# Performance work log

Measured on AMD Instinct MI355X. Metric: run time of the kernel, lower is better.

Reference implementation:

```python
import jax, jax.numpy as jnp
import numpy as np

NEG_INF = -9e15  # matches the source's -9000000000000000.0 mask fill
ALPHA = 0.2      # leaky_relu negative slope


def setup_inputs() -> dict:
    key = jax.random.key(0)
    k1, k2, k3, k4 = jax.random.split(key, 4)
    B, N, C_IN, C_OUT, H = 2, 2048, 128, 128, 16
    c = C_OUT // H  # 8 per-head features; equals H//2 so source's a-slice is consistent
    node_feats = jax.random.normal(k1, (B, N, C_IN), dtype=jnp.float32)
    # random 0/1 adjacency with self-loops
    adj = jax.random.randint(k2, (B, N, N), 0, 2).astype(jnp.float32)
    adj = jnp.maximum(adj, jnp.eye(N, dtype=jnp.float32)[None])
    # glorot-uniform-ish params
    W = jax.random.normal(k3, (C_IN, H * c), dtype=jnp.float32) * np.sqrt(2.0 / (C_IN + H * c))
    b = jnp.zeros((H * c,), dtype=jnp.float32)
    a = jax.random.normal(k4, (H, 2 * c), dtype=jnp.float32) * np.sqrt(2.0 / (H + 2 * c))
    return {"node_feats": node_feats, "adj_matrix": adj, "W": W, "b": b, "a": a}


def reference(node_feats, adj_matrix, W, b, a):
    B, N = node_feats.shape[:2]
    H = a.shape[0]
    c = a.shape[1] // 2
    # projection + split into heads: [B, N, H, c]
    h = (node_feats @ W + b).reshape(B, N, H, c)
    # additive attention halves (source slices a along last axis)
    logit_parent = jnp.einsum('bnhc,hc->bnh', h, a[:, :c])
    logit_child = jnp.einsum('bnhc,hc->bnh', h, a[:, c:])
    # dense broadcast-add logits: [B, N(i), N(j), H]
    attn_logits = logit_parent[:, :, None, :] + logit_child[:, None, :, :]
    attn_logits = jax.nn.leaky_relu(attn_logits, negative_slope=ALPHA)
    attn_logits = jnp.where(adj_matrix[..., None] == 1.0, attn_logits, NEG_INF)
    attn_probs = jax.nn.softmax(attn_logits, axis=2)  # over source nodes j
    out = jnp.einsum('bijh,bjhc->bihc', attn_probs, h)
    out = out.reshape(B, N, H * c)  # concat_heads=True
    return out, adj_matrix
```

## Files before the change

### kernel.cpp

```cpp
#include <hip/hip_runtime.h>
#include <hip/hip_bf16.h>


#define B_   2
#define N_   2048
#define CIN_ 128
#define H_   16

typedef _Float16 h2  __attribute__((ext_vector_type(2)));
typedef _Float16 v8h __attribute__((ext_vector_type(8)));
typedef float    v4f __attribute__((ext_vector_type(4)));

#define SC6 0.015625f

__device__ inline h2 pk_f16(float a, float b) {
  return __builtin_bit_cast(h2, __builtin_amdgcn_cvt_pkrtz(a, b));
}
__device__ inline unsigned as_u32(h2 v) { return __builtin_bit_cast(unsigned, v); }
__device__ inline h2 as_h2(unsigned u) { return __builtin_bit_cast(h2, u); }

__device__ inline unsigned mask4(float4 f) {
  unsigned r = (unsigned)f.x | ((unsigned)f.y << 8) |
               ((unsigned)f.z << 16) | ((unsigned)f.w << 24);
  return (r << 8) - r;
}

__global__ __launch_bounds__(128) void proj_kernel(
    const float* __restrict__ nf, const float* __restrict__ W,
    const float* __restrict__ bias, const float* __restrict__ a,
    unsigned* __restrict__ hQ, unsigned* __restrict__ qI,
    float* __restrict__ lpT, unsigned* __restrict__ ones) {
  const int row0 = blockIdx.x * 4;
  const int t    = threadIdx.x;
  if (blockIdx.x == 0) {
    ones[t] = 0x3C003C00u; ones[t + 128] = 0x3C003C00u;
    ones[t + 256] = 0x3C003C00u; ones[t + 384] = 0x3C003C00u;
  }
  __shared__ float sNf[4][CIN_];
  ((float4*)&sNf[0][0])[t] = ((const float4*)(nf + (long)row0 * CIN_))[t];
  __syncthreads();
  float acc[4];
  const float bv = bias[t];
#pragma unroll
  for (int r = 0; r < 4; ++r) acc[r] = bv;
#pragma unroll 8
  for (int k = 0; k < CIN_; ++k) {
    const float w = W[k * 128 + t];
#pragma unroll
    for (int r = 0; r < 4; ++r) acc[r] = fmaf(sNf[r][k], w, acc[r]);
  }
  const int h = t >> 3, kc = t & 7;
  const int b = row0 >> 11, n0 = row0 & (N_ - 1);
  const int bh = b * H_ + h;
  const int cdw = n0 >> 1;
  uint2 hv;
  hv.x = as_u32(pk_f16(acc[0], acc[1]));
  hv.y = as_u32(pk_f16(acc[2], acc[3]));
  *(uint2*)(hQ + ((long)(bh * 8 + kc)) * (N_ / 2) + cdw) = hv;

  const float ap = a[h * 16 + kc], ac = a[h * 16 + 8 + kc];
  float lpv[4], lcv[4];
#pragma unroll
  for (int r = 0; r < 4; ++r) {
    float x = acc[r] * ap, y = acc[r] * ac;
#pragma unroll
    for (int s = 1; s < 8; s <<= 1) {
      x += __shfl_xor(x, s);
      y += __shfl_xor(y, s);
    }
    lpv[r] = x; lcv[r] = y;
  }
  if (kc == 0) {
    float4 l0 = {lpv[0], lpv[1], lpv[2], lpv[3]};
    *(float4*)(lpT + (long)bh * N_ + n0) = l0;
    uint2 q1, q2;
    q1.x = as_u32(pk_f16(__expf(lcv[0]) * SC6, __expf(lcv[1]) * SC6));
    q1.y = as_u32(pk_f16(__expf(lcv[2]) * SC6, __expf(lcv[3]) * SC6));
    q2.x = as_u32(pk_f16(__expf(0.2f * lcv[0]) * SC6, __expf(0.2f * lcv[1]) * SC6));
    q2.y = as_u32(pk_f16(__expf(0.2f * lcv[2]) * SC6, __expf(0.2f * lcv[3]) * SC6));
    const int addr = bh * 2048 + (cdw >> 4) * 32 + ((cdw >> 2) & 3) * 8;
    const int off  = cdw & 3;
    *(uint2*)(qI + addr + off)     = q1;
    *(uint2*)(qI + addr + 4 + off) = q2;
  }
}

__global__ __launch_bounds__(256) void attn_kernel(
    const float* __restrict__ adj, const unsigned* __restrict__ hQ,
    const unsigned* __restrict__ qI, const float* __restrict__ lpT,
    const unsigned* __restrict__ ones, float* __restrict__ out,
    float* __restrict__ adj_out) {
  const int hg   = blockIdx.x & 3;
  const int it   = (blockIdx.x >> 2) & 63;
  const int b    = blockIdx.x >> 8;
  const int i0   = it * 32;
  const int t    = threadIdx.x;
  const int w    = t >> 6;
  const int lane = t & 63;
  const int m    = lane & 15;
  const int q    = lane >> 4;
  const int h    = hg * 4 + w;
  const int bh   = b * H_ + h;

  __shared__ uint2 sAm[8192];

  const int  tm = t & 15, tq = t >> 4;
  const long abase = ((long)(b * N_) + i0) * N_;

  float4 fa[2][4], fb[2][4];
  auto STAGE_LOAD = [&](int ss) {
#pragma unroll
    for (int u = 0; u < 2; ++u)
#pragma unroll
      for (int k = 0; k < 4; ++k) {
        const int qc  = ss * 64 + k * 16 + tq;
        const int col = qc * 8;
        const float* ap = adj + abase + (long)(u * 16 + tm) * N_ + col;
        fa[u][k] = *(const float4*)(ap);
        fb[u][k] = *(const float4*)(ap + 4);
      }
  };
  auto STAGE_WRITE = [&](int ss) {
    const bool docopy = (ss == hg);
#pragma unroll
    for (int u = 0; u < 2; ++u)
#pragma unroll
      for (int k = 0; k < 4; ++k) {
        uint2 mv;
        mv.x = mask4(fa[u][k]); mv.y = mask4(fb[u][k]);
        sAm[u * 4096 + ss * 1024 + k * 256 + t] = mv;
        if (docopy) {
          const int qc  = ss * 64 + k * 16 + tq;
          const int col = qc * 8;
          float* op = adj_out + abase + (long)(u * 16 + tm) * N_ + col;
          *(float4*)(op)     = fa[u][k];
          *(float4*)(op + 4) = fb[u][k];
        }
      }
  };

  const float lpa = lpT[(long)bh * N_ + i0 + m];
  const float lpb = lpT[(long)bh * N_ + i0 + 16 + m];
  const float e1a = __expf(lpa) * SC6, e2a = __expf(0.2f * lpa) * SC6;
  const float e1b = __expf(lpb) * SC6, e2b = __expf(0.2f * lpb) * SC6;
  const h2 P1a = pk_f16(e1a, e1a), P2a = pk_f16(e2a, e2a);
  const h2 P1b = pk_f16(e1b, e1b), P2b = pk_f16(e2b, e2b);

  const unsigned* qp = qI + bh * 2048 + q * 8;
  const unsigned hmask = (m < 8) ? ~0u : 0u;
  const unsigned* hp = (m < 8)
      ? hQ + ((long)(bh * 8 + m)) * (N_ / 2) + q * 4
      : ones + q * 4;

  uint4 bq1[2], bq2[2], bhq[2];
  bq1[0] = *(const uint4*)(qp);       bq2[0] = *(const uint4*)(qp + 4);
  bq1[1] = *(const uint4*)(qp + 32);  bq2[1] = *(const uint4*)(qp + 36);
  bhq[0] = *(const uint4*)(hp);
  bhq[1] = *(const uint4*)(hp + (16 & hmask));

  v4f acc0 = {0.f, 0.f, 0.f, 0.f};
  v4f acc1 = {0.f, 0.f, 0.f, 0.f};

  STAGE_LOAD(0);
  STAGE_WRITE(0);
  __syncthreads();

  for (int s = 0; s < 4; ++s) {
    if (s < 3) STAGE_LOAD(s + 1);
#pragma unroll
    for (int cc = 0; cc < 16; ++cc) {
      const int ch = s * 16 + cc;
      const int p  = ch & 1;
      const uint4 nq1 = *(const uint4*)(qp + (ch + 2) * 32);
      const uint4 nq2 = *(const uint4*)(qp + (ch + 2) * 32 + 4);
      const uint4 nhq = *(const uint4*)(hp + (((ch + 2) * 16) & hmask));

      const uint2 Mv0 = sAm[ch * 64 + lane];
      const uint2 Mv1 = sAm[4096 + ch * 64 + lane];
      const unsigned m0a = __builtin_amdgcn_perm(Mv0.x, Mv0.x, 0x01010000u);
      const unsigned m0b = __builtin_amdgcn_perm(Mv0.x, Mv0.x, 0x03030202u);
      const unsigned m0c = __builtin_amdgcn_perm(Mv0.y, Mv0.y, 0x01010000u);
      const unsigned m0d = __builtin_amdgcn_perm(Mv0.y, Mv0.y, 0x03030202u);
      const unsigned m1a = __builtin_amdgcn_perm(Mv1.x, Mv1.x, 0x01010000u);
      const unsigned m1b = __builtin_amdgcn_perm(Mv1.x, Mv1.x, 0x03030202u);
      const unsigned m1c = __builtin_amdgcn_perm(Mv1.y, Mv1.y, 0x01010000u);
      const unsigned m1d = __builtin_amdgcn_perm(Mv1.y, Mv1.y, 0x03030202u);

      const uint4 q1 = bq1[p], q2 = bq2[p];
      const h2 Q1x = as_h2(q1.x), Q1y = as_h2(q1.y), Q1z = as_h2(q1.z), Q1w = as_h2(q1.w);
      const h2 Q2x = as_h2(q2.x), Q2y = as_h2(q2.y), Q2z = as_h2(q2.z), Q2w = as_h2(q2.w);
      const v8h bf = __builtin_bit_cast(v8h, bhq[p]);

      const uint4 af0 = {
        as_u32(__builtin_elementwise_max(P1a * Q1x, P2a * Q2x)) & m0a,
        as_u32(__builtin_elementwise_max(P1a * Q1y, P2a * Q2y)) & m0b,
        as_u32(__builtin_elementwise_max(P1a * Q1z, P2a * Q2z)) & m0c,
        as_u32(__builtin_elementwise_max(P1a * Q1w, P2a * Q2w)) & m0d};
      acc0 = __builtin_amdgcn_mfma_f32_16x16x32_f16(
          __builtin_bit_cast(v8h, af0), bf, acc0, 0, 0, 0);
      const uint4 af1 = {
        as_u32(__builtin_elementwise_max(P1b * Q1x, P2b * Q2x)) & m1a,
        as_u32(__builtin_elementwise_max(P1b * Q1y, P2b * Q2y)) & m1b,
        as_u32(__builtin_elementwise_max(P1b * Q1z, P2b * Q2z)) & m1c,
        as_u32(__builtin_elementwise_max(P1b * Q1w, P2b * Q2w)) & m1d};
      acc1 = __builtin_amdgcn_mfma_f32_16x16x32_f16(
          __builtin_bit_cast(v8h, af1), bf, acc1, 0, 0, 0);

      bq1[p] = nq1; bq2[p] = nq2; bhq[p] = nhq;
    }
    if (s < 3) { STAGE_WRITE(s + 1); __syncthreads(); }
  }

#pragma unroll
  for (int u = 0; u < 2; ++u) {
    const v4f av = u ? acc1 : acc0;
#pragma unroll
    for (int r = 0; r < 4; ++r) {
      const float sden = __shfl(av[r], (lane & 48) | 8);
      if (m < 8) {
        const long gi = ((long)(b * N_ + i0 + u * 16 + q * 4 + r)) * H_ + h;
        out[gi * 8 + m] = av[r] / sden;
      }
    }
  }
}

extern "C" void kernel_launch(void* const* d_in, const int* in_sizes, int n_in,
                              void* d_out, int out_size, void* d_ws, size_t ws_size,
                              hipStream_t stream) {
  const float* nf   = (const float*)d_in[0];
  const float* adj  = (const float*)d_in[1];
  const float* W    = (const float*)d_in[2];
  const float* bias = (const float*)d_in[3];
  const float* a    = (const float*)d_in[4];

  float* out     = (float*)d_out;
  float* adj_out = out + (long)B_ * N_ * H_ * 8;

  unsigned* ws   = (unsigned*)d_ws;
  unsigned* hQ   = ws;
  unsigned* qI   = ws + 262144;
  float*    lpT  = (float*)(ws + 327680);
  unsigned* ones = ws + 393216;

  hipLaunchKernelGGL(proj_kernel, dim3(B_ * N_ / 4), dim3(128), 0, stream,
                     nf, W, bias, a, hQ, qI, lpT, ones);
  hipLaunchKernelGGL(attn_kernel, dim3(B_ * 64 * 4), dim3(256), 0,
                     stream, adj, hQ, qI, lpT, ones, out, adj_out);
}
```

Baseline: 139.5 us.

## Halve row tile per block, double grid, double-buffer adjacency masks with swizzled block order

Each block now handles 16 query rows instead of 32, so the grid grows from 512 to 1024 blocks and shared memory shrinks from 64KB to 8KB. Adjacency masks are staged in 8 smaller double-buffered chunks instead of holding the whole strip. Block indices are remapped so that neighbouring launch slots land on different row tiles, and launch bounds ask for 4 blocks per CU. The intent is higher occupancy and better latency hiding on the adjacency stream. The cost is that the per-node q/h operand loads and exp setup are now amortised over half as many rows, and there are more barriers per block.

```diff
diff --git a/kernel.cpp b/kernel.cpp
--- a/kernel.cpp
+++ b/kernel.cpp
@@ -85,15 +85,16 @@
   }
 }
 
-__global__ __launch_bounds__(256) void attn_kernel(
+__global__ __launch_bounds__(256, 4) void attn_kernel(
     const float* __restrict__ adj, const unsigned* __restrict__ hQ,
     const unsigned* __restrict__ qI, const float* __restrict__ lpT,
     const unsigned* __restrict__ ones, float* __restrict__ out,
     float* __restrict__ adj_out) {
-  const int hg   = blockIdx.x & 3;
-  const int it   = (blockIdx.x >> 2) & 63;
-  const int b    = blockIdx.x >> 8;
-  const int i0   = it * 32;
+  const int L    = (blockIdx.x & 7) * 128 + (blockIdx.x >> 3);
+  const int hg   = L & 3;
+  const int it   = (L >> 2) & 127;
+  const int b    = L >> 9;
+  const int i0   = it * 16;
   const int t    = threadIdx.x;
   const int w    = t >> 6;
   const int lane = t & 63;
@@ -102,49 +103,39 @@
   const int h    = hg * 4 + w;
   const int bh   = b * H_ + h;
 
-  __shared__ uint2 sAm[8192];
-
-  const int  tm = t & 15, tq = t >> 4;
-  const long abase = ((long)(b * N_) + i0) * N_;
-
-  float4 fa[2][4], fb[2][4];
+  __shared__ uint2 sAm[1024];
+
+  const int  tm = t & 15, cg = t >> 4;
+  const int  chl = cg >> 1, qh = (cg & 1) * 2;
+  const long abase = ((long)(b * N_) + i0 + tm) * N_ + cg * 16;
+  const bool owner_even = (hg == 0) | (hg == 1) | (hg == 2) | (hg == 3);
+
+  float4 f0, f1, f2, f3;
   auto STAGE_LOAD = [&](int ss) {
-#pragma unroll
-    for (int u = 0; u < 2; ++u)
-#pragma unroll
-      for (int k = 0; k < 4; ++k) {
-        const int qc  = ss * 64 + k * 16 + tq;
-        const int col = qc * 8;
-        const float* ap = adj + abase + (long)(u * 16 + tm) * N_ + col;
-        fa[u][k] = *(const float4*)(ap);
-        fb[u][k] = *(const float4*)(ap + 4);
-      }
+    const float* ap = adj + abase + ss * 256;
+    f0 = *(const float4*)(ap);
+    f1 = *(const float4*)(ap + 4);
+    f2 = *(const float4*)(ap + 8);
+    f3 = *(const float4*)(ap + 12);
   };
   auto STAGE_WRITE = [&](int ss) {
-    const bool docopy = (ss == hg);
-#pragma unroll
-    for (int u = 0; u < 2; ++u)
-#pragma unroll
-      for (int k = 0; k < 4; ++k) {
-        uint2 mv;
-        mv.x = mask4(fa[u][k]); mv.y = mask4(fb[u][k]);
-        sAm[u * 4096 + ss * 1024 + k * 256 + t] = mv;
-        if (docopy) {
-          const int qc  = ss * 64 + k * 16 + tq;
-          const int col = qc * 8;
-          float* op = adj_out + abase + (long)(u * 16 + tm) * N_ + col;
-          *(float4*)(op)     = fa[u][k];
-          *(float4*)(op + 4) = fb[u][k];
-        }
-      }
+    const int buf = (ss & 1) * 512;
+    uint2 mv0; mv0.x = mask4(f0); mv0.y = mask4(f1);
+    uint2 mv1; mv1.x = mask4(f2); mv1.y = mask4(f3);
+    sAm[buf + chl * 64 + qh * 16 + tm]       = mv0;
+    sAm[buf + chl * 64 + (qh + 1) * 16 + tm] = mv1;
+    if (hg == (ss & 3)) {
+      float* op = adj_out + abase + ss * 256;
+      *(float4*)(op)      = f0;
+      *(float4*)(op + 4)  = f1;
+      *(float4*)(op + 8)  = f2;
+      *(float4*)(op + 12) = f3;
+    }
   };
 
-  const float lpa = lpT[(long)bh * N_ + i0 + m];
-  const float lpb = lpT[(long)bh * N_ + i0 + 16 + m];
-  const float e1a = __expf(lpa) * SC6, e2a = __expf(0.2f * lpa) * SC6;
-  const float e1b = __expf(lpb) * SC6, e2b = __expf(0.2f * lpb) * SC6;
-  const h2 P1a = pk_f16(e1a, e1a), P2a = pk_f16(e2a, e2a);
-  const h2 P1b = pk_f16(e1b, e1b), P2b = pk_f16(e2b, e2b);
+  const float lp  = lpT[(long)bh * N_ + i0 + m];
+  const float e1  = __expf(lp) * SC6, e2 = __expf(0.2f * lp) * SC6;
+  const h2 P1 = pk_f16(e1, e1), P2 = pk_f16(e2, e2);
 
   const unsigned* qp = qI + bh * 2048 + q * 8;
   const unsigned hmask = (m < 8) ? ~0u : 0u;
@@ -158,71 +149,53 @@
   bhq[0] = *(const uint4*)(hp);
   bhq[1] = *(const uint4*)(hp + (16 & hmask));
 
-  v4f acc0 = {0.f, 0.f, 0.f, 0.f};
-  v4f acc1 = {0.f, 0.f, 0.f, 0.f};
+  v4f acc = {0.f, 0.f, 0.f, 0.f};
 
   STAGE_LOAD(0);
   STAGE_WRITE(0);
   __syncthreads();
 
-  for (int s = 0; s < 4; ++s) {
-    if (s < 3) STAGE_LOAD(s + 1);
-#pragma unroll
-    for (int cc = 0; cc < 16; ++cc) {
-      const int ch = s * 16 + cc;
+  for (int s = 0; s < 8; ++s) {
+    if (s < 7) STAGE_LOAD(s + 1);
+    const int buf = (s & 1) * 512;
+#pragma unroll
+    for (int cc = 0; cc < 8; ++cc) {
+      const int ch = s * 8 + cc;
       const int p  = ch & 1;
       const uint4 nq1 = *(const uint4*)(qp + (ch + 2) * 32);
       const uint4 nq2 = *(const uint4*)(qp + (ch + 2) * 32 + 4);
       const uint4 nhq = *(const uint4*)(hp + (((ch + 2) * 16) & hmask));
 
-      const uint2 Mv0 = sAm[ch * 64 + lane];
-      const uint2 Mv1 = sAm[4096 + ch * 64 + lane];
-      const unsigned m0a = __builtin_amdgcn_perm(Mv0.x, Mv0.x, 0x01010000u);
-      const unsigned m0b = __builtin_amdgcn_perm(Mv0.x, Mv0.x, 0x03030202u);
-      const unsigned m0c = __builtin_amdgcn_perm(Mv0.y, Mv0.y, 0x01010000u);
-      const unsigned m0d = __builtin_amdgcn_perm(Mv0.y, Mv0.y, 0x03030202u);
-      const unsigned m1a = __builtin_amdgcn_perm(Mv1.x, Mv1.x, 0x01010000u);
-      const unsigned m1b = __builtin_amdgcn_perm(Mv1.x, Mv1.x, 0x03030202u);
-      const unsigned m1c = __builtin_amdgcn_perm(Mv1.y, Mv1.y, 0x01010000u);
-      const unsigned m1d = __builtin_amdgcn_perm(Mv1.y, Mv1.y, 0x03030202u);
+      const uint2 Mv = sAm[buf + cc * 64 + lane];
+      const unsigned ma = __builtin_amdgcn_perm(Mv.x, Mv.x, 0x01010000u);
+      const unsigned mb = __builtin_amdgcn_perm(Mv.x, Mv.x, 0x03030202u);
+      const unsigned mc = __builtin_amdgcn_perm(Mv.y, Mv.y, 0x01010000u);
+      const unsigned md = __builtin_amdgcn_perm(Mv.y, Mv.y, 0x03030202u);
 
       const uint4 q1 = bq1[p], q2 = bq2[p];
-      const h2 Q1x = as_h2(q1.x), Q1y = as_h2(q1.y), Q1z = as_h2(q1.z), Q1w = as_h2(q1.w);
-      const h2 Q2x = as_h2(q2.x), Q2y = as_h2(q2.y), Q2z = as_h2(q2.z), Q2w = as_h2(q2.w);
       const v8h bf = __builtin_bit_cast(v8h, bhq[p]);
-
-      const uint4 af0 = {
-        as_u32(__builtin_elementwise_max(P1a * Q1x, P2a * Q2x)) & m0a,
-        as_u32(__builtin_elementwise_max(P1a * Q1y, P2a * Q2y)) & m0b,
-        as_u32(__builtin_elementwise_max(P1a * Q1z, P2a * Q2z)) & m0c,
-        as_u32(__builtin_elementwise_max(P1a * Q1w, P2a * Q2w)) & m0d};
-      acc0 = __builtin_amdgcn_mfma_f32_16x16x32_f16(
-          __builtin_bit_cast(v8h, af0), bf, acc0, 0, 0, 0);
-      const uint4 af1 = {
-        as_u32(__builtin_elementwise_max(P1b * Q1x, P2b * Q2x)) & m1a,
-        as_u32(__builtin_elementwise_max(P1b * Q1y, P2b * Q2y)) & m1b,
-        as_u32(__builtin_elementwise_max(P1b * Q1z, P2b * Q2z)) & m1c,
-        as_u32(__builtin_elementwise_max(P1b * Q1w, P2b * Q2w)) & m1d};
-      acc1 = __builtin_amdgcn_mfma_f32_16x16x32_f16(
-          __builtin_bit_cast(v8h, af1), bf, acc1, 0, 0, 0);
+      const uint4 af = {
+        as_u32(__builtin_elementwise_max(P1 * as_h2(q1.x), P2 * as_h2(q2.x))) & ma,
+        as_u32(__builtin_elementwise_max(P1 * as_h2(q1.y), P2 * as_h2(q2.y))) & mb,
+        as_u32(__builtin_elementwise_max(P1 * as_h2(q1.z), P2 * as_h2(q2.z))) & mc,
+        as_u32(__builtin_elementwise_max(P1 * as_h2(q1.w), P2 * as_h2(q2.w))) & md};
+      acc = __builtin_amdgcn_mfma_f32_16x16x32_f16(
+          __builtin_bit_cast(v8h, af), bf, acc, 0, 0, 0);
 
       bq1[p] = nq1; bq2[p] = nq2; bhq[p] = nhq;
     }
-    if (s < 3) { STAGE_WRITE(s + 1); __syncthreads(); }
-  }
-
-#pragma unroll
-  for (int u = 0; u < 2; ++u) {
-    const v4f av = u ? acc1 : acc0;
-#pragma unroll
-    for (int r = 0; r < 4; ++r) {
-      const float sden = __shfl(av[r], (lane & 48) | 8);
-      if (m < 8) {
-        const long gi = ((long)(b * N_ + i0 + u * 16 + q * 4 + r)) * H_ + h;
-        out[gi * 8 + m] = av[r] / sden;
-      }
-    }
-  }
+    if (s < 7) { STAGE_WRITE(s + 1); __syncthreads(); }
+  }
+
+#pragma unroll
+  for (int r = 0; r < 4; ++r) {
+    const float sden = __shfl(acc[r], (lane & 48) | 8);
+    if (m < 8) {
+      const long gi = ((long)(b * N_ + i0 + q * 4 + r)) * H_ + h;
+      out[gi * 8 + m] = acc[r] / sden;
+    }
+  }
+  (void)owner_even;
 }
 
 extern "C" void kernel_launch(void* const* d_in, const int* in_sizes, int n_in,
@@ -245,6 +218,6 @@
 
   hipLaunchKernelGGL(proj_kernel, dim3(B_ * N_ / 4), dim3(128), 0, stream,
                      nf, W, bias, a, hQ, qI, lpT, ones);
-  hipLaunchKernelGGL(attn_kernel, dim3(B_ * 64 * 4), dim3(256), 0,
+  hipLaunchKernelGGL(attn_kernel, dim3(1024), dim3(256), 0,
                      stream, adj, hQ, qI, lpT, ones, out, adj_out);
 }
```

New measurement: 146.5 us. 5.1% more time.

## Double-buffer adjacency and query tiles in LDS with interleaved prefetch

Applied to the files above, without the earlier changes.

The attention kernel now double-buffers both the adjacency mask and the per-head query-exponent vectors in shared memory. Loads for the next 512-column chunk are split into four sub-stages spread across the MFMA loop, with sched barriers to keep them in place. It also adds an occupancy hint of two blocks per CU and remaps block indices so neighbouring blocks are spread across XCDs. The aim is to hide global load latency behind compute and to cut register pressure from the per-thread query prefetch, at the cost of an extra __syncthreads per chunk and more LDS traffic.

```diff
diff --git a/kernel.cpp b/kernel.cpp
--- a/kernel.cpp
+++ b/kernel.cpp
@@ -85,58 +85,64 @@
   }
 }
 
-__global__ __launch_bounds__(256) void attn_kernel(
+__global__ __launch_bounds__(256, 2) void attn_kernel(
     const float* __restrict__ adj, const unsigned* __restrict__ hQ,
     const unsigned* __restrict__ qI, const float* __restrict__ lpT,
     const unsigned* __restrict__ ones, float* __restrict__ out,
     float* __restrict__ adj_out) {
-  const int hg   = blockIdx.x & 3;
-  const int it   = (blockIdx.x >> 2) & 63;
-  const int b    = blockIdx.x >> 8;
-  const int i0   = it * 32;
-  const int t    = threadIdx.x;
-  const int w    = t >> 6;
-  const int lane = t & 63;
-  const int m    = lane & 15;
-  const int q    = lane >> 4;
-  const int h    = hg * 4 + w;
-  const int bh   = b * H_ + h;
-
-  __shared__ uint2 sAm[8192];
-
-  const int  tm = t & 15, tq = t >> 4;
-  const long abase = ((long)(b * N_) + i0) * N_;
-
-  float4 fa[2][4], fb[2][4];
-  auto STAGE_LOAD = [&](int ss) {
-#pragma unroll
-    for (int u = 0; u < 2; ++u)
-#pragma unroll
-      for (int k = 0; k < 4; ++k) {
-        const int qc  = ss * 64 + k * 16 + tq;
-        const int col = qc * 8;
-        const float* ap = adj + abase + (long)(u * 16 + tm) * N_ + col;
-        fa[u][k] = *(const float4*)(ap);
-        fb[u][k] = *(const float4*)(ap + 4);
-      }
-  };
-  auto STAGE_WRITE = [&](int ss) {
-    const bool docopy = (ss == hg);
-#pragma unroll
-    for (int u = 0; u < 2; ++u)
-#pragma unroll
-      for (int k = 0; k < 4; ++k) {
-        uint2 mv;
-        mv.x = mask4(fa[u][k]); mv.y = mask4(fb[u][k]);
-        sAm[u * 4096 + ss * 1024 + k * 256 + t] = mv;
-        if (docopy) {
-          const int qc  = ss * 64 + k * 16 + tq;
-          const int col = qc * 8;
-          float* op = adj_out + abase + (long)(u * 16 + tm) * N_ + col;
-          *(float4*)(op)     = fa[u][k];
-          *(float4*)(op + 4) = fb[u][k];
-        }
-      }
+  const int L  = (blockIdx.x & 7) * 64 + (blockIdx.x >> 3);
+  const int hg = L & 3;
+  const int it = (L >> 2) & 63;
+  const int b  = L >> 8;
+  const int i0 = it * 32;
+  const int t = threadIdx.x, w = t >> 6, lane = t & 63;
+  const int m = lane & 15, q = lane >> 4;
+  const int h = hg * 4 + w, bh = b * H_ + h;
+
+  __shared__ unsigned sQ[2][2048];
+  __shared__ uint2    sAm[2][2048];
+
+  const int srow = t & 31, su = srow >> 4, smm = srow & 15;
+  const int scg  = t >> 5;
+  const long arow = ((long)(b * N_) + i0 + srow) * N_;
+  const unsigned* qbase =
+      qI + (long)(b * H_ + hg * 4 + w) * 2048 + lane * 8;
+
+  float4 f0, f1, f2, f3;
+  uint4  s0, s1;
+
+  auto SQ_LOAD = [&](int jqn) {
+    const unsigned* sp = qbase + jqn * 512;
+    s0 = *(const uint4*)(sp);
+    s1 = *(const uint4*)(sp + 4);
+  };
+  auto SQ_WRITE = [&](int nb) {
+    unsigned* dp = &sQ[nb][w * 512 + lane * 8];
+    *(uint4*)(dp)     = s0;
+    *(uint4*)(dp + 4) = s1;
+  };
+  auto ADJ_LOAD = [&](int jqn, int sb) {
+    const float* ap = adj + arow + jqn * 512 + sb * 128 + scg * 16;
+    f0 = *(const float4*)(ap);
+    f1 = *(const float4*)(ap + 4);
+    f2 = *(const float4*)(ap + 8);
+    f3 = *(const float4*)(ap + 12);
+  };
+  auto ADJ_WRITE = [&](int jqn, int sb, int nb) {
+    uint2 mva, mvb;
+    mva.x = mask4(f0); mva.y = mask4(f1);
+    mvb.x = mask4(f2); mvb.y = mask4(f3);
+    const int col = sb * 128 + scg * 16;
+    const int idx = su * 1024 + (col >> 5) * 64 + ((col & 31) >> 3) * 16 + smm;
+    sAm[nb][idx]      = mva;
+    sAm[nb][idx + 16] = mvb;
+    if (hg == sb) {
+      float* op = adj_out + arow + jqn * 512 + col;
+      *(float4*)(op)      = f0;
+      *(float4*)(op + 4)  = f1;
+      *(float4*)(op + 8)  = f2;
+      *(float4*)(op + 12) = f3;
+    }
   };
 
   const float lpa = lpT[(long)bh * N_ + i0 + m];
@@ -146,37 +152,56 @@
   const h2 P1a = pk_f16(e1a, e1a), P2a = pk_f16(e2a, e2a);
   const h2 P1b = pk_f16(e1b, e1b), P2b = pk_f16(e2b, e2b);
 
-  const unsigned* qp = qI + bh * 2048 + q * 8;
   const unsigned hmask = (m < 8) ? ~0u : 0u;
   const unsigned* hp = (m < 8)
       ? hQ + ((long)(bh * 8 + m)) * (N_ / 2) + q * 4
       : ones + q * 4;
-
-  uint4 bq1[2], bq2[2], bhq[2];
-  bq1[0] = *(const uint4*)(qp);       bq2[0] = *(const uint4*)(qp + 4);
-  bq1[1] = *(const uint4*)(qp + 32);  bq2[1] = *(const uint4*)(qp + 36);
+  uint4 bhq[2];
   bhq[0] = *(const uint4*)(hp);
   bhq[1] = *(const uint4*)(hp + (16 & hmask));
 
   v4f acc0 = {0.f, 0.f, 0.f, 0.f};
   v4f acc1 = {0.f, 0.f, 0.f, 0.f};
 
-  STAGE_LOAD(0);
-  STAGE_WRITE(0);
+  SQ_LOAD(0);  ADJ_LOAD(0, 0);
+  SQ_WRITE(0); ADJ_WRITE(0, 0, 0);
+  ADJ_LOAD(0, 1); ADJ_WRITE(0, 1, 0);
+  ADJ_LOAD(0, 2); ADJ_WRITE(0, 2, 0);
+  ADJ_LOAD(0, 3); ADJ_WRITE(0, 3, 0);
   __syncthreads();
 
-  for (int s = 0; s < 4; ++s) {
-    if (s < 3) STAGE_LOAD(s + 1);
+  for (int jq = 0; jq < 4; ++jq) {
+    const int buf = jq & 1, nbuf = buf ^ 1;
+    const unsigned* sqb = &sQ[buf][w * 512 + q * 8];
+    const uint2*    smb = &sAm[buf][0];
 #pragma unroll
     for (int cc = 0; cc < 16; ++cc) {
-      const int ch = s * 16 + cc;
-      const int p  = ch & 1;
-      const uint4 nq1 = *(const uint4*)(qp + (ch + 2) * 32);
-      const uint4 nq2 = *(const uint4*)(qp + (ch + 2) * 32 + 4);
-      const uint4 nhq = *(const uint4*)(hp + (((ch + 2) * 16) & hmask));
-
-      const uint2 Mv0 = sAm[ch * 64 + lane];
-      const uint2 Mv1 = sAm[4096 + ch * 64 + lane];
+      const int p = cc & 1;
+      const int gn = ((jq * 16 + cc + 2) & 63) * 16;
+      const uint4 nhq = *(const uint4*)(hp + (gn & hmask));
+
+      if (jq < 3) {
+        if (cc == 0) {
+          SQ_LOAD(jq + 1); ADJ_LOAD(jq + 1, 0);
+          __builtin_amdgcn_sched_barrier(0);
+        } else if (cc == 4) {
+          SQ_WRITE(nbuf); ADJ_WRITE(jq + 1, 0, nbuf); ADJ_LOAD(jq + 1, 1);
+          __builtin_amdgcn_sched_barrier(0);
+        } else if (cc == 8) {
+          ADJ_WRITE(jq + 1, 1, nbuf); ADJ_LOAD(jq + 1, 2);
+          __builtin_amdgcn_sched_barrier(0);
+        } else if (cc == 12) {
+          ADJ_WRITE(jq + 1, 2, nbuf); ADJ_LOAD(jq + 1, 3);
+          __builtin_amdgcn_sched_barrier(0);
+        } else if (cc == 15) {
+          ADJ_WRITE(jq + 1, 3, nbuf);
+        }
+      }
+
+      const uint4 q1 = *(const uint4*)(sqb + cc * 32);
+      const uint4 q2 = *(const uint4*)(sqb + cc * 32 + 4);
+      const uint2 Mv0 = smb[cc * 64 + lane];
+      const uint2 Mv1 = smb[1024 + cc * 64 + lane];
       const unsigned m0a = __builtin_amdgcn_perm(Mv0.x, Mv0.x, 0x01010000u);
       const unsigned m0b = __builtin_amdgcn_perm(Mv0.x, Mv0.x, 0x03030202u);
       const unsigned m0c = __builtin_amdgcn_perm(Mv0.y, Mv0.y, 0x01010000u);
@@ -186,7 +211,6 @@
       const unsigned m1c = __builtin_amdgcn_perm(Mv1.y, Mv1.y, 0x01010000u);
       const unsigned m1d = __builtin_amdgcn_perm(Mv1.y, Mv1.y, 0x03030202u);
 
-      const uint4 q1 = bq1[p], q2 = bq2[p];
       const h2 Q1x = as_h2(q1.x), Q1y = as_h2(q1.y), Q1z = as_h2(q1.z), Q1w = as_h2(q1.w);
       const h2 Q2x = as_h2(q2.x), Q2y = as_h2(q2.y), Q2z = as_h2(q2.z), Q2w = as_h2(q2.w);
       const v8h bf = __builtin_bit_cast(v8h, bhq[p]);
@@ -206,9 +230,9 @@
       acc1 = __builtin_amdgcn_mfma_f32_16x16x32_f16(
           __builtin_bit_cast(v8h, af1), bf, acc1, 0, 0, 0);
 
-      bq1[p] = nq1; bq2[p] = nq2; bhq[p] = nhq;
-    }
-    if (s < 3) { STAGE_WRITE(s + 1); __syncthreads(); }
+      bhq[p] = nhq;
+    }
+    __syncthreads();
   }
 
 #pragma unroll
@@ -245,6 +269,6 @@
 
   hipLaunchKernelGGL(proj_kernel, dim3(B_ * N_ / 4), dim3(128), 0, stream,
                      nf, W, bias, a, hQ, qI, lpT, ones);
-  hipLaunchKernelGGL(attn_kernel, dim3(B_ * 64 * 4), dim3(256), 0,
+  hipLaunchKernelGGL(attn_kernel, dim3(512), dim3(256), 0,
                      stream, adj, hQ, qI, lpT, ones, out, adj_out);
 }
```

Result: faster. 128.6 us (-7.8%).

## Split adjacency masking into separate prep kernel and stream masks from global

Applied to the files above, without the earlier changes.

Moves adjacency reading, the adj_out copy and the byte-mask packing into a new prep_kernel that writes a compact mask buffer to workspace. The attention kernel no longer uses shared memory or __syncthreads; it streams mask words from global memory with a four-deep register prefetch and runs at two blocks per CU. Block indices are also swizzled so that neighbouring blocks are spread across XCDs. The cost is an extra kernel launch and an extra global write and read of the mask buffer, in exchange for removing shared-memory staging and barriers from the attention loop.

```diff
diff --git a/kernel.cpp b/kernel.cpp
--- a/kernel.cpp
+++ b/kernel.cpp
@@ -85,59 +85,39 @@
   }
 }
 
-__global__ __launch_bounds__(256) void attn_kernel(
-    const float* __restrict__ adj, const unsigned* __restrict__ hQ,
-    const unsigned* __restrict__ qI, const float* __restrict__ lpT,
-    const unsigned* __restrict__ ones, float* __restrict__ out,
-    float* __restrict__ adj_out) {
-  const int hg   = blockIdx.x & 3;
-  const int it   = (blockIdx.x >> 2) & 63;
-  const int b    = blockIdx.x >> 8;
-  const int i0   = it * 32;
-  const int t    = threadIdx.x;
-  const int w    = t >> 6;
-  const int lane = t & 63;
-  const int m    = lane & 15;
-  const int q    = lane >> 4;
-  const int h    = hg * 4 + w;
-  const int bh   = b * H_ + h;
-
-  __shared__ uint2 sAm[8192];
-
-  const int  tm = t & 15, tq = t >> 4;
-  const long abase = ((long)(b * N_) + i0) * N_;
-
-  float4 fa[2][4], fb[2][4];
-  auto STAGE_LOAD = [&](int ss) {
-#pragma unroll
-    for (int u = 0; u < 2; ++u)
-#pragma unroll
-      for (int k = 0; k < 4; ++k) {
-        const int qc  = ss * 64 + k * 16 + tq;
-        const int col = qc * 8;
-        const float* ap = adj + abase + (long)(u * 16 + tm) * N_ + col;
-        fa[u][k] = *(const float4*)(ap);
-        fb[u][k] = *(const float4*)(ap + 4);
-      }
-  };
-  auto STAGE_WRITE = [&](int ss) {
-    const bool docopy = (ss == hg);
-#pragma unroll
-    for (int u = 0; u < 2; ++u)
-#pragma unroll
-      for (int k = 0; k < 4; ++k) {
-        uint2 mv;
-        mv.x = mask4(fa[u][k]); mv.y = mask4(fb[u][k]);
-        sAm[u * 4096 + ss * 1024 + k * 256 + t] = mv;
-        if (docopy) {
-          const int qc  = ss * 64 + k * 16 + tq;
-          const int col = qc * 8;
-          float* op = adj_out + abase + (long)(u * 16 + tm) * N_ + col;
-          *(float4*)(op)     = fa[u][k];
-          *(float4*)(op + 4) = fb[u][k];
-        }
-      }
-  };
+__global__ __launch_bounds__(128) void prep_kernel(
+    const float* __restrict__ adj, float* __restrict__ adj_out,
+    uint2* __restrict__ mks) {
+  const int Lp  = (blockIdx.x & 7) * 64 + (blockIdx.x >> 3);
+  const int b   = Lp >> 8, it = (Lp >> 2) & 63, qtr = Lp & 3;
+  const int t   = threadIdx.x;
+  const int u   = t & 1, q = (t >> 1) & 3, m = (t >> 3) & 15;
+  const int row = it * 32 + u * 16 + m;
+  const long rbase = ((long)(b * N_) + row) * N_;
+  uint2* mb = mks + ((long)(b * 64 + it)) * 8192;
+#pragma unroll 4
+  for (int cc = 0; cc < 16; ++cc) {
+    const int ch  = qtr * 16 + cc;
+    const int col = ch * 32 + q * 8;
+    const float4 fa = *(const float4*)(adj + rbase + col);
+    const float4 fb = *(const float4*)(adj + rbase + col + 4);
+    *(float4*)(adj_out + rbase + col)     = fa;
+    *(float4*)(adj_out + rbase + col + 4) = fb;
+    uint2 mv; mv.x = mask4(fa); mv.y = mask4(fb);
+    mb[ch * 128 + (m * 4 + q) * 2 + u] = mv;
+  }
+}
+
+__global__ __launch_bounds__(256, 2) void attn_kernel(
+    const unsigned* __restrict__ hQ, const unsigned* __restrict__ qI,
+    const float* __restrict__ lpT, const unsigned* __restrict__ ones,
+    const uint4* __restrict__ mks, float* __restrict__ out) {
+  const int L  = (blockIdx.x & 7) * 64 + (blockIdx.x >> 3);
+  const int hg = L & 3, it = (L >> 2) & 63, b = L >> 8;
+  const int i0 = it * 32;
+  const int t = threadIdx.x, w = t >> 6, lane = t & 63;
+  const int m = lane & 15, q = lane >> 4;
+  const int h = hg * 4 + w, bh = b * H_ + h;
 
   const float lpa = lpT[(long)bh * N_ + i0 + m];
   const float lpb = lpT[(long)bh * N_ + i0 + 16 + m];
@@ -146,13 +126,16 @@
   const h2 P1a = pk_f16(e1a, e1a), P2a = pk_f16(e2a, e2a);
   const h2 P1b = pk_f16(e1b, e1b), P2b = pk_f16(e2b, e2b);
 
+  const uint4* mp = mks + ((long)(b * 64 + it)) * 4096 + (m * 4 + q);
   const unsigned* qp = qI + bh * 2048 + q * 8;
   const unsigned hmask = (m < 8) ? ~0u : 0u;
   const unsigned* hp = (m < 8)
       ? hQ + ((long)(bh * 8 + m)) * (N_ / 2) + q * 4
       : ones + q * 4;
 
-  uint4 bq1[2], bq2[2], bhq[2];
+  uint4 bmk[4], bq1[2], bq2[2], bhq[2];
+#pragma unroll
+  for (int d = 0; d < 4; ++d) bmk[d] = mp[d * 64];
   bq1[0] = *(const uint4*)(qp);       bq2[0] = *(const uint4*)(qp + 4);
   bq1[1] = *(const uint4*)(qp + 32);  bq2[1] = *(const uint4*)(qp + 36);
   bhq[0] = *(const uint4*)(hp);
@@ -161,22 +144,19 @@
   v4f acc0 = {0.f, 0.f, 0.f, 0.f};
   v4f acc1 = {0.f, 0.f, 0.f, 0.f};
 
-  STAGE_LOAD(0);
-  STAGE_WRITE(0);
-  __syncthreads();
-
-  for (int s = 0; s < 4; ++s) {
-    if (s < 3) STAGE_LOAD(s + 1);
+  for (int t16 = 0; t16 < 4; ++t16) {
 #pragma unroll
     for (int cc = 0; cc < 16; ++cc) {
-      const int ch = s * 16 + cc;
-      const int p  = ch & 1;
-      const uint4 nq1 = *(const uint4*)(qp + (ch + 2) * 32);
-      const uint4 nq2 = *(const uint4*)(qp + (ch + 2) * 32 + 4);
-      const uint4 nhq = *(const uint4*)(hp + (((ch + 2) * 16) & hmask));
-
-      const uint2 Mv0 = sAm[ch * 64 + lane];
-      const uint2 Mv1 = sAm[4096 + ch * 64 + lane];
+      const int ch = t16 * 16 + cc;
+      const int p2 = ch & 1, p4 = ch & 3;
+      const uint4 nmk = mp[((ch + 4) & 63) * 64];
+      const int qn = ((ch + 2) & 63) * 32;
+      const uint4 nq1 = *(const uint4*)(qp + qn);
+      const uint4 nq2 = *(const uint4*)(qp + qn + 4);
+      const uint4 nhq = *(const uint4*)(hp + ((((ch + 2) & 63) * 16) & hmask));
+
+      const uint2 Mv0 = {bmk[p4].x, bmk[p4].y};
+      const uint2 Mv1 = {bmk[p4].z, bmk[p4].w};
       const unsigned m0a = __builtin_amdgcn_perm(Mv0.x, Mv0.x, 0x01010000u);
       const unsigned m0b = __builtin_amdgcn_perm(Mv0.x, Mv0.x, 0x03030202u);
       const unsigned m0c = __builtin_amdgcn_perm(Mv0.y, Mv0.y, 0x01010000u);
@@ -186,10 +166,10 @@
       const unsigned m1c = __builtin_amdgcn_perm(Mv1.y, Mv1.y, 0x01010000u);
       const unsigned m1d = __builtin_amdgcn_perm(Mv1.y, Mv1.y, 0x03030202u);
 
-      const uint4 q1 = bq1[p], q2 = bq2[p];
+      const uint4 q1 = bq1[p2], q2 = bq2[p2];
       const h2 Q1x = as_h2(q1.x), Q1y = as_h2(q1.y), Q1z = as_h2(q1.z), Q1w = as_h2(q1.w);
       const h2 Q2x = as_h2(q2.x), Q2y = as_h2(q2.y), Q2z = as_h2(q2.z), Q2w = as_h2(q2.w);
-      const v8h bf = __builtin_bit_cast(v8h, bhq[p]);
+      const v8h bf = __builtin_bit_cast(v8h, bhq[p2]);
 
       const uint4 af0 = {
         as_u32(__builtin_elementwise_max(P1a * Q1x, P2a * Q2x)) & m0a,
@@ -206,9 +186,8 @@
       acc1 = __builtin_amdgcn_mfma_f32_16x16x32_f16(
           __builtin_bit_cast(v8h, af1), bf, acc1, 0, 0, 0);
 
-      bq1[p] = nq1; bq2[p] = nq2; bhq[p] = nhq;
+      bmk[p4] = nmk; bq1[p2] = nq1; bq2[p2] = nq2; bhq[p2] = nhq;
     }
-    if (s < 3) { STAGE_WRITE(s + 1); __syncthreads(); }
   }
 
 #pragma unroll
@@ -242,9 +221,12 @@
   unsigned* qI   = ws + 262144;
   float*    lpT  = (float*)(ws + 327680);
   unsigned* ones = ws + 393216;
+  unsigned* mks  = ws + 393728;
 
   hipLaunchKernelGGL(proj_kernel, dim3(B_ * N_ / 4), dim3(128), 0, stream,
                      nf, W, bias, a, hQ, qI, lpT, ones);
-  hipLaunchKernelGGL(attn_kernel, dim3(B_ * 64 * 4), dim3(256), 0,
-                     stream, adj, hQ, qI, lpT, ones, out, adj_out);
-}
+  hipLaunchKernelGGL(prep_kernel, dim3(512), dim3(128), 0, stream,
+                     adj, adj_out, (uint2*)mks);
+  hipLaunchKernelGGL(attn_kernel, dim3(512), dim3(256), 0, stream,
+                     hQ, qI, lpT, ones, (const uint4*)mks, out);
+}
```

Result: slower. 164.2 us (+17.7%).
